# Kernel tuning notes

Measured on AMD Instinct MI355X. Metric: run time of the kernel, lower is better.

## Reference

```python
import jax, jax.numpy as jnp
import numpy as np

# dims
B, S, IN, H = 8, 2048, 512, 512
# biophysical constants (from module defaults / buffers)
DT = 0.1
TAU_M, TAU_ADAPT = 20.0, 100.0
V_REST, V_THRESH, V_RESET = -65.0, -50.0, -65.0
ADAPT_A, ADAPT_B = 0.5, 0.1
E_NA, E_K, E_L = 50.0, -77.0, -54.4
# HH gate initial values (IonicCurrents lazy init)
M0, H0, N0 = 0.05, 0.6, 0.32


def setup_inputs() -> dict:
    key = jax.random.key(0)
    k1, k2 = jax.random.split(key)
    x = jax.random.normal(k1, (B, S, IN), dtype=jnp.float32)
    W = jax.random.normal(k2, (H, IN), dtype=jnp.float32) * 0.01  # SynapticPlasticity.weights
    return {
        "x": x,
        "W": W,
        "g_Na": jnp.float32(120.0),
        "g_K": jnp.float32(36.0),
        "g_L": jnp.float32(0.3),
    }


def reference(x, W, g_Na, g_K, g_L):
    """BiologicalSNNLayer.forward, first call (all internal states at init).

    post_spikes = psp0 = 0 and traces start at 0, so the STDP dw is exactly 0
    on this call; psp = 0*decay + syn_input = syn_input.
    """
    dt = jnp.float32(DT)
    # SynapticPlasticity forward output: F.linear(x, W)
    syn = jnp.einsum("bsi,hi->bsh", x, W)  # [B,S,H]
    psp = syn
    V = psp
    # Hodgkin-Huxley gating: one Euler step from initial gate values
    am = 0.1 * (V + 40.0) / (1.0 - jnp.exp(-(V + 40.0) / 10.0))
    bm = 4.0 * jnp.exp(-(V + 65.0) / 18.0)
    ah = 0.07 * jnp.exp(-(V + 65.0) / 20.0)
    bh = 1.0 / (1.0 + jnp.exp(-(V + 35.0) / 10.0))
    an = 0.01 * (V + 55.0) / (1.0 - jnp.exp(-(V + 55.0) / 10.0))
    bn = 0.125 * jnp.exp(-(V + 65.0) / 80.0)
    m = M0 + dt * (am * (1.0 - M0) - bm * M0)
    h = H0 + dt * (ah * (1.0 - H0) - bh * H0)
    n = N0 + dt * (an * (1.0 - N0) - bn * N0)
    I_ion = (
        g_Na * m ** 3 * h * (V - E_NA)
        + g_K * n ** 4 * (V - E_K)
        + g_L * (V - E_L)
    )
    # Adaptive LIF (all hidden_size neurons share params -> vectorized over last dim)
    I_in = I_ion + psp
    # v0 = V_REST, w0 = 0 -> dv = I_in * dt/tau_m
    v_new = V_REST + I_in * (dt / TAU_M)
    spike = (v_new >= V_THRESH).astype(jnp.float32)
    w_new = (ADAPT_A * (v_new - V_REST) + ADAPT_B * spike) * (dt / TAU_ADAPT)
    v_rs = jnp.where(spike > 0.5, jnp.float32(V_RESET), v_new)
    return spike, v_rs, w_new
```

## Files before the change

### kernel.cpp

```cpp
#include <hip/hip_runtime.h>
#include <hip/hip_bf16.h>
#include <math.h>

typedef __bf16 bf16x8 __attribute__((ext_vector_type(8)));
typedef float  f32x4  __attribute__((ext_vector_type(4)));

#define M_DIM 16384
#define N_DIM 512
#define K_DIM 512
#define TBL_N 1024

__device__ inline bf16x8 cvt8(float4 a, float4 b) {
    bf16x8 r;
    r[0] = (__bf16)a.x; r[1] = (__bf16)a.y; r[2] = (__bf16)a.z; r[3] = (__bf16)a.w;
    r[4] = (__bf16)b.x; r[5] = (__bf16)b.y; r[6] = (__bf16)b.z; r[7] = (__bf16)b.w;
    return r;
}

__global__ __launch_bounds__(256, 4)
void snn_fused_kernel(const float* __restrict__ x, const float* __restrict__ W,
                      const float* __restrict__ gNa_p, const float* __restrict__ gK_p,
                      const float* __restrict__ gL_p, float* __restrict__ out)
{
    __shared__ __bf16 sW[64 * 64];
    __shared__ __bf16 sX[128 * 64];
    __shared__ float  tbl[TBL_N + 1];

    const int tid = threadIdx.x;

    const int id   = blockIdx.x;
    const int xcd  = id & 7;
    const int slot = id >> 3;
    const int bm   = xcd * 16 + (slot >> 3);
    const int bn   = slot & 7;

    const int wv   = tid >> 6;
    const int ln   = tid & 63;
    const int lr   = ln & 15;
    const int quad = ln >> 4;

    const int rw  = ln >> 3;
    const int ch  = ln & 7;
    const int chx = (ch ^ rw) * 8;

    const float* wSrc = W + ((long)bn * 64 + 16 * wv + rw) * K_DIM + chx;
    const float* xSrc = x + ((long)bm * 128 + 32 * wv + rw) * K_DIM + chx;
    __bf16* wDst = sW + (16 * wv + rw) * 64 + ch * 8;
    __bf16* xDst = sX + (32 * wv + rw) * 64 + ch * 8;

    float4 pw[2][2], px[4][2];
    #pragma unroll
    for (int j = 0; j < 2; ++j) {
        pw[j][0] = *(const float4*)(wSrc + (long)(8 * j) * K_DIM);
        pw[j][1] = *(const float4*)(wSrc + (long)(8 * j) * K_DIM + 4);
    }
    #pragma unroll
    for (int j = 0; j < 4; ++j) {
        px[j][0] = *(const float4*)(xSrc + (long)(8 * j) * K_DIM);
        px[j][1] = *(const float4*)(xSrc + (long)(8 * j) * K_DIM + 4);
    }

    {
        const float gNa = *gNa_p, gK = *gK_p, gL = *gL_p;
        for (int i = tid; i <= TBL_N; i += 256) {
            const float V = -4.0f + (8.0f / TBL_N) * i;
            const float am = 0.1f * (V + 40.0f) / (1.0f - expf(-(V + 40.0f) * 0.1f));
            const float bm_ = 4.0f * expf(-(V + 65.0f) * (1.0f / 18.0f));
            const float ah = 0.07f * expf(-(V + 65.0f) * 0.05f);
            const float bh = 1.0f / (1.0f + expf(-(V + 35.0f) * 0.1f));
            const float an = 0.01f * (V + 55.0f) / (1.0f - expf(-(V + 55.0f) * 0.1f));
            const float bn_ = 0.125f * expf(-(V + 65.0f) * 0.0125f);
            const float m = 0.05f + 0.1f * (am * 0.95f - bm_ * 0.05f);
            const float h = 0.60f + 0.1f * (ah * 0.40f - bh * 0.60f);
            const float n = 0.32f + 0.1f * (an * 0.68f - bn_ * 0.32f);
            tbl[i] = gNa * m * m * m * h * (V - 50.0f)
                   + gK * (n * n) * (n * n) * (V + 77.0f)
                   + gL * (V + 54.4f) + V;
        }
    }

    f32x4 acc[4][2] = {};

    for (int t = 0; t < 8; ++t) {
        const int nk = (t + 1) * 64;
        #pragma unroll
        for (int j = 0; j < 2; ++j) {
            float4 a = pw[j][0], b = pw[j][1];
            if (t < 7) {
                pw[j][0] = *(const float4*)(wSrc + (long)(8 * j) * K_DIM + nk);
                pw[j][1] = *(const float4*)(wSrc + (long)(8 * j) * K_DIM + nk + 4);
            }
            *(bf16x8*)(wDst + 8 * j * 64) = cvt8(a, b);
        }
        #pragma unroll
        for (int j = 0; j < 4; ++j) {
            float4 a = px[j][0], b = px[j][1];
            if (t < 7) {
                px[j][0] = *(const float4*)(xSrc + (long)(8 * j) * K_DIM + nk);
                px[j][1] = *(const float4*)(xSrc + (long)(8 * j) * K_DIM + nk + 4);
            }
            *(bf16x8*)(xDst + 8 * j * 64) = cvt8(a, b);
        }
        __syncthreads();
        #pragma unroll
        for (int kk = 0; kk < 2; ++kk) {
            const int cidx = quad + 4 * kk;
            const int sl   = (cidx ^ (lr & 7)) * 8;
            bf16x8 aw[4], bx[2];
            #pragma unroll
            for (int f = 0; f < 4; ++f)
                aw[f] = *(const bf16x8*)(sW + (f * 16 + lr) * 64 + sl);
            #pragma unroll
            for (int g = 0; g < 2; ++g)
                bx[g] = *(const bf16x8*)(sX + (32 * wv + g * 16 + lr) * 64 + sl);
            #pragma unroll
            for (int f = 0; f < 4; ++f)
                #pragma unroll
                for (int g = 0; g < 2; ++g)
                    acc[f][g] = __builtin_amdgcn_mfma_f32_16x16x32_bf16(
                        aw[f], bx[g], acc[f][g], 0, 0, 0);
        }
        __syncthreads();
    }

    float* outS = out;
    float* outV = out + (long)M_DIM * N_DIM;
    float* outW = out + 2L * M_DIM * N_DIM;

    #pragma unroll
    for (int f = 0; f < 4; ++f) {
        const int gn4 = bn * 64 + f * 16 + quad * 4;
        #pragma unroll
        for (int g = 0; g < 2; ++g) {
            const long gm  = (long)bm * 128 + 32 * wv + g * 16 + lr;
            const long idx = gm * N_DIM + gn4;
            f32x4 vS, vV, vW;
            #pragma unroll
            for (int i = 0; i < 4; ++i) {
                const float V = acc[f][g][i];
                float u = (V + 4.0f) * (TBL_N / 8.0f);
                u = fminf(fmaxf(u, 0.0f), (float)TBL_N - 0.001f);
                const int   iu = (int)u;
                const float fr = u - (float)iu;
                const float I_in = tbl[iu] + fr * (tbl[iu + 1] - tbl[iu]);
                const float v_new = -65.0f + I_in * 0.005f;
                const float spike = (v_new >= -50.0f) ? 1.0f : 0.0f;
                vS[i] = spike;
                vW[i] = (0.5f * (v_new + 65.0f) + 0.1f * spike) * 0.001f;
                vV[i] = (spike > 0.5f) ? -65.0f : v_new;
            }
            *(f32x4*)(outS + idx) = vS;
            *(f32x4*)(outV + idx) = vV;
            *(f32x4*)(outW + idx) = vW;
        }
    }
}

extern "C" void kernel_launch(void* const* d_in, const int* in_sizes, int n_in,
                              void* d_out, int out_size, void* d_ws, size_t ws_size,
                              hipStream_t stream) {
    const float* x   = (const float*)d_in[0];
    const float* W   = (const float*)d_in[1];
    const float* gNa = (const float*)d_in[2];
    const float* gK  = (const float*)d_in[3];
    const float* gL  = (const float*)d_in[4];
    float* out = (float*)d_out;
    (void)d_ws; (void)ws_size;

    hipLaunchKernelGGL(snn_fused_kernel, dim3(1024), dim3(256), 0, stream,
                       x, W, gNa, gK, gL, out);
}
```

Before: 178.8 us.

## Double-buffer LDS tiles to drop one barrier per K step

Splits the shared-memory W and x tiles into two buffers. The next tile is converted and stored into the alternate buffer after the current tile's MFMAs, which leaves one __syncthreads per iteration instead of two. The register prefetch now runs two tiles ahead. LDS use roughly doubles, so the launch bound drops from 4 to 3 blocks per SIMD, which can reduce occupancy.

```diff
diff --git a/kernel.cpp b/kernel.cpp
--- a/kernel.cpp
+++ b/kernel.cpp
@@ -17,13 +17,13 @@
     return r;
 }
 
-__global__ __launch_bounds__(256, 4)
+__global__ __launch_bounds__(256, 3)
 void snn_fused_kernel(const float* __restrict__ x, const float* __restrict__ W,
                       const float* __restrict__ gNa_p, const float* __restrict__ gK_p,
                       const float* __restrict__ gL_p, float* __restrict__ out)
 {
-    __shared__ __bf16 sW[64 * 64];
-    __shared__ __bf16 sX[128 * 64];
+    __shared__ __bf16 sW[2][64 * 64];
+    __shared__ __bf16 sX[2][128 * 64];
     __shared__ float  tbl[TBL_N + 1];
 
     const int tid = threadIdx.x;
@@ -45,10 +45,10 @@
 
     const float* wSrc = W + ((long)bn * 64 + 16 * wv + rw) * K_DIM + chx;
     const float* xSrc = x + ((long)bm * 128 + 32 * wv + rw) * K_DIM + chx;
-    __bf16* wDst = sW + (16 * wv + rw) * 64 + ch * 8;
-    __bf16* xDst = sX + (32 * wv + rw) * 64 + ch * 8;
+    const int wOff = (16 * wv + rw) * 64 + ch * 8;
+    const int xOff = (32 * wv + rw) * 64 + ch * 8;
 
-    float4 pw[2][2], px[4][2];
+    float4 px[4][2], pw[2][2];
     #pragma unroll
     for (int j = 0; j < 2; ++j) {
         pw[j][0] = *(const float4*)(wSrc + (long)(8 * j) * K_DIM);
@@ -79,29 +79,26 @@
         }
     }
 
+    #pragma unroll
+    for (int j = 0; j < 2; ++j) {
+        float4 a = pw[j][0], b = pw[j][1];
+        pw[j][0] = *(const float4*)(wSrc + (long)(8 * j) * K_DIM + 64);
+        pw[j][1] = *(const float4*)(wSrc + (long)(8 * j) * K_DIM + 64 + 4);
+        *(bf16x8*)(&sW[0][wOff + 8 * j * 64]) = cvt8(a, b);
+    }
+    #pragma unroll
+    for (int j = 0; j < 4; ++j) {
+        float4 a = px[j][0], b = px[j][1];
+        px[j][0] = *(const float4*)(xSrc + (long)(8 * j) * K_DIM + 64);
+        px[j][1] = *(const float4*)(xSrc + (long)(8 * j) * K_DIM + 64 + 4);
+        *(bf16x8*)(&sX[0][xOff + 8 * j * 64]) = cvt8(a, b);
+    }
+    __syncthreads();
+
     f32x4 acc[4][2] = {};
 
     for (int t = 0; t < 8; ++t) {
-        const int nk = (t + 1) * 64;
-        #pragma unroll
-        for (int j = 0; j < 2; ++j) {
-            float4 a = pw[j][0], b = pw[j][1];
-            if (t < 7) {
-                pw[j][0] = *(const float4*)(wSrc + (long)(8 * j) * K_DIM + nk);
-                pw[j][1] = *(const float4*)(wSrc + (long)(8 * j) * K_DIM + nk + 4);
-            }
-            *(bf16x8*)(wDst + 8 * j * 64) = cvt8(a, b);
-        }
-        #pragma unroll
-        for (int j = 0; j < 4; ++j) {
-            float4 a = px[j][0], b = px[j][1];
-            if (t < 7) {
-                px[j][0] = *(const float4*)(xSrc + (long)(8 * j) * K_DIM + nk);
-                px[j][1] = *(const float4*)(xSrc + (long)(8 * j) * K_DIM + nk + 4);
-            }
-            *(bf16x8*)(xDst + 8 * j * 64) = cvt8(a, b);
-        }
-        __syncthreads();
+        const int cur = t & 1;
         #pragma unroll
         for (int kk = 0; kk < 2; ++kk) {
             const int cidx = quad + 4 * kk;
@@ -109,10 +106,10 @@
             bf16x8 aw[4], bx[2];
             #pragma unroll
             for (int f = 0; f < 4; ++f)
-                aw[f] = *(const bf16x8*)(sW + (f * 16 + lr) * 64 + sl);
+                aw[f] = *(const bf16x8*)(&sW[cur][(f * 16 + lr) * 64 + sl]);
             #pragma unroll
             for (int g = 0; g < 2; ++g)
-                bx[g] = *(const bf16x8*)(sX + (32 * wv + g * 16 + lr) * 64 + sl);
+                bx[g] = *(const bf16x8*)(&sX[cur][(32 * wv + g * 16 + lr) * 64 + sl]);
             #pragma unroll
             for (int f = 0; f < 4; ++f)
                 #pragma unroll
@@ -120,7 +117,28 @@
                     acc[f][g] = __builtin_amdgcn_mfma_f32_16x16x32_bf16(
                         aw[f], bx[g], acc[f][g], 0, 0, 0);
         }
-        __syncthreads();
+        if (t < 7) {
+            const int nk = (t + 2) * 64;
+            #pragma unroll
+            for (int j = 0; j < 2; ++j) {
+                float4 a = pw[j][0], b = pw[j][1];
+                if (t < 6) {
+                    pw[j][0] = *(const float4*)(wSrc + (long)(8 * j) * K_DIM + nk);
+                    pw[j][1] = *(const float4*)(wSrc + (long)(8 * j) * K_DIM + nk + 4);
+                }
+                *(bf16x8*)(&sW[cur ^ 1][wOff + 8 * j * 64]) = cvt8(a, b);
+            }
+            #pragma unroll
+            for (int j = 0; j < 4; ++j) {
+                float4 a = px[j][0], b = px[j][1];
+                if (t < 6) {
+                    px[j][0] = *(const float4*)(xSrc + (long)(8 * j) * K_DIM + nk);
+                    px[j][1] = *(const float4*)(xSrc + (long)(8 * j) * K_DIM + nk + 4);
+                }
+                *(bf16x8*)(&sX[cur ^ 1][xOff + 8 * j * 64]) = cvt8(a, b);
+            }
+            __syncthreads();
+        }
     }
 
     float* outS = out;
```

Measured after the change: 158.5 us. 1.13x faster.
